# Optimization experiments

Measured on AMD Instinct MI355X. Metric: run time of the kernel, lower is better.

The kernel has to match this reference:

```python
import jax, jax.numpy as jnp
import numpy as np

TEMPERATURE = 0.07
TIME_THRESH = 5.0 * 1e6  # microseconds


def setup_inputs() -> dict:
    key = jax.random.key(0)
    k1, k2, k3 = jax.random.split(key, 3)
    B, D = 8192, 512
    desc = jax.random.normal(k1, (B, D), dtype=jnp.float32)
    desc = desc / jnp.linalg.norm(desc, axis=-1, keepdims=True)  # module expects normalized descriptors
    seq_ids = jax.random.randint(k2, (B,), 0, 64, dtype=jnp.int64)
    time_mid = jax.random.randint(k3, (B,), 0, 20_000_000, dtype=jnp.int64)
    return {"descriptors": desc, "seq_ids": seq_ids, "time_mid": time_mid}


def reference(descriptors, seq_ids, time_mid):
    B = descriptors.shape[0]
    # [B, B] temperature-scaled cosine similarities
    logits = jnp.matmul(descriptors, descriptors.T) / TEMPERATURE

    eye = jnp.eye(B, dtype=bool)
    same_seq = seq_ids[:, None] == seq_ids[None, :]
    close_time = jnp.abs(time_mid[:, None] - time_mid[None, :]).astype(jnp.float32) < TIME_THRESH
    pos_mask = same_seq & close_time & ~eye  # positives
    offdiag = ~eye                            # positives + negatives = denominator support

    # denominator per row i: log sum_{j != i} exp(logits[i, j])
    denom_lse = jax.nn.logsumexp(jnp.where(offdiag, logits, -jnp.inf), axis=1)  # [B]

    # per positive pair (i, j): -log( exp(l_ij) / denom_i ) = denom_lse_i - l_ij
    pair_loss = jnp.where(pos_mask, denom_lse[:, None] - logits, 0.0)
    num_pos = jnp.sum(pos_mask)
    loss = jnp.sum(pair_loss) / jnp.maximum(num_pos, 1).astype(pair_loss.dtype)
    return loss
```

## Files before the change

kernel.cpp:

```cpp
#include <hip/hip_runtime.h>
#include <math.h>

#define TILE 128

typedef __attribute__((ext_vector_type(4))) float f32x4;
typedef __attribute__((ext_vector_type(2))) long long llong2;

#define INV_T    14.285714285714286f
#define K2C      20.60992915f
#define K2C8     0.32203014296875f
#define INV_T64  0.22321428571428573f
#define TIME_THR 5000000

__device__ __forceinline__ unsigned pack_bf16x2(float lo, float hi) {
  unsigned a = __float_as_uint(lo);
  unsigned b = __float_as_uint(hi);
  a = (a + 0x7FFFu + ((a >> 16) & 1u)) >> 16;
  b = (b + 0x7FFFu + ((b >> 16) & 1u)) & 0xFFFF0000u;
  return b | a;
}

__device__ __forceinline__ unsigned f32_to_e4m3(float x) {
  unsigned u = __float_as_uint(x);
  unsigned s = (u >> 24) & 0x80u;
  int e = (int)((u >> 23) & 0xffu) - 127;
  unsigned m = u & 0x7fffffu;
  if (e < -9) return s;
  if (e < -6) {
    int sh = 20 + (-6 - e);
    unsigned full = (1u << 23) | m;
    unsigned q = full >> sh;
    unsigned rem = full & ((1u << sh) - 1u);
    unsigned half = 1u << (sh - 1);
    if (rem > half || (rem == half && (q & 1u))) q++;
    return s | q;
  }
  unsigned q = m >> 20;
  unsigned rem = m & 0xfffffu;
  if (rem > 0x80000u || (rem == 0x80000u && (q & 1u))) q++;
  int ee = e;
  if (q == 8u) { q = 0u; ee++; }
  if (ee > 8 || (ee == 8 && q == 7u)) return s | 0x7eu;
  return s | (unsigned)((ee + 7) << 3) | q;
}

__device__ __forceinline__ void gl_lds16(const void* g, void* l) {
  __builtin_amdgcn_global_load_lds(
      (const __attribute__((address_space(1))) unsigned int*)g,
      (__attribute__((address_space(3))) unsigned int*)l, 16, 0, 0);
}

template <int MODE>
__device__ __forceinline__ void infonce_body(
    const float* __restrict__ desc, const unsigned char* __restrict__ desc8,
    const int* __restrict__ seq, const int* __restrict__ tmid,
    float* __restrict__ p_se, float* __restrict__ p_ps,
    float* __restrict__ p_pc, int B, int D, int NB) {
  __shared__ __align__(16) unsigned char lA8[3][TILE][64];
  __shared__ __align__(16) unsigned char lB8[3][TILE][64];
  __shared__ int mseq_r[TILE], mtim_r[TILE], mseq_c[TILE], mtim_c[TILE];

  const int T = NB * (NB + 1) / 2;
  int t = blockIdx.x;
  if ((T & 7) == 0) t = (t & 7) * (T >> 3) + (t >> 3);
  float fn = (float)NB + 0.5f;
  int r = (int)(fn - sqrtf(fmaxf(fn * fn - 2.0f * (float)t, 0.0f)));
  if (r < 0) r = 0;
  if (r > NB - 1) r = NB - 1;
  auto Sf = [NB](int rr) { return rr * NB - ((rr * (rr - 1)) >> 1); };
  while (r > 0 && Sf(r) > t) --r;
  while (r < NB - 1 && Sf(r + 1) <= t) ++r;
  const int rb = r;
  const int cb = rb + (t - Sf(rb));
  const bool upper = (cb != rb);

  const int row0 = rb * TILE;
  const int col0 = cb * TILE;

  const int tid = threadIdx.x;
  const int l = tid & 63;
  const int w = tid >> 6;
  const int wrow = (w >> 1) << 6;
  const int wcol = (w & 1) << 6;
  const int lr = l & 15;
  const int kg = l >> 4;

  if (tid < TILE) {
    mseq_r[tid] = seq[row0 + tid];
    mtim_r[tid] = tmid[row0 + tid];
    mseq_c[tid] = seq[col0 + tid];
    mtim_c[tid] = tmid[col0 + tid];
  }

  f32x4 acc[4][4];
#pragma unroll
  for (int m = 0; m < 4; ++m)
#pragma unroll
    for (int n = 0; n < 4; ++n) acc[m][n] = (f32x4){0.f, 0.f, 0.f, 0.f};

  const int NT = D >> 6;

  const int sr = tid >> 3;
  const int sc = tid & 7;

  if (MODE == 2) {
    const unsigned char* pa =
        desc8 + (size_t)(row0 + (tid >> 2)) * D + (tid & 3) * 16;
    const unsigned char* pb =
        desc8 + (size_t)(col0 + (tid >> 2)) * D + (tid & 3) * 16;
    const size_t rstep = (size_t)64 * D;

    auto stage = [&](int bu_, int tt) {
      const int off = tt << 6;
      gl_lds16(pa + off, (char*)&lA8[bu_][0][0] + tid * 16);
      gl_lds16(pa + off + rstep, (char*)&lA8[bu_][0][0] + 4096 + tid * 16);
      gl_lds16(pb + off, (char*)&lB8[bu_][0][0] + tid * 16);
      gl_lds16(pb + off + rstep, (char*)&lB8[bu_][0][0] + 4096 + tid * 16);
    };

    __builtin_amdgcn_sched_barrier(0);
    stage(0, 0);
    if (NT > 1) stage(1, 1);
    __builtin_amdgcn_sched_barrier(0);

    int bu = 0;
    for (int ts = 0; ts < NT; ++ts) {
      if (ts + 2 < NT) {
        int sbu = bu + 2;
        if (sbu >= 3) sbu -= 3;
        stage(sbu, ts + 2);
        __builtin_amdgcn_sched_barrier(0);
        asm volatile("s_waitcnt vmcnt(8)" ::: "memory");
      } else if (ts + 1 < NT) {
        asm volatile("s_waitcnt vmcnt(4)" ::: "memory");
      } else {
        asm volatile("s_waitcnt vmcnt(0)" ::: "memory");
      }
      __builtin_amdgcn_sched_barrier(0);
      __builtin_amdgcn_s_barrier();
      __builtin_amdgcn_sched_barrier(0);

      llong2 av[4], bv[4];
#pragma unroll
      for (int m = 0; m < 4; ++m) {
        const int row = wrow + (m << 4) + lr;
        const int ch = kg ^ ((row + (row >> 2)) & 3);
        av[m] = *reinterpret_cast<const llong2*>(&lA8[bu][row][ch << 4]);
      }
#pragma unroll
      for (int n = 0; n < 4; ++n) {
        const int row = wcol + (n << 4) + lr;
        const int ch = kg ^ ((row + (row >> 2)) & 3);
        bv[n] = *reinterpret_cast<const llong2*>(&lB8[bu][row][ch << 4]);
      }
      __builtin_amdgcn_sched_barrier(0);
      asm volatile("s_waitcnt lgkmcnt(0)" ::: "memory");
      __builtin_amdgcn_sched_barrier(0);
      __builtin_amdgcn_s_setprio(1);
#pragma unroll
      for (int kk = 0; kk < 2; ++kk)
#pragma unroll
        for (int m = 0; m < 4; ++m)
#pragma unroll
          for (int n = 0; n < 4; ++n)
            acc[m][n] = __builtin_amdgcn_mfma_f32_16x16x32_fp8_fp8(
                av[m][kk], bv[n][kk], acc[m][n], 0, 0, 0);
      __builtin_amdgcn_s_setprio(0);
      __builtin_amdgcn_sched_barrier(0);
      __builtin_amdgcn_s_barrier();
      bu = bu == 2 ? 0 : bu + 1;
    }
    __syncthreads();
  } else {
    __shared__ __align__(16) unsigned short lAw[TILE][64];
    __shared__ __align__(16) unsigned short lBw[TILE][64];
    typedef __attribute__((ext_vector_type(8))) short short8v;
    for (int k0 = 0; k0 < D; k0 += 64) {
      __syncthreads();
#pragma unroll
      for (int p = 0; p < 4; ++p) {
        const int rr = (p << 5) + sr;
        const float* gA = desc + (size_t)(row0 + rr) * D + k0 + (sc << 3);
        const float4 fa0 = *reinterpret_cast<const float4*>(gA);
        const float4 fa1 = *reinterpret_cast<const float4*>(gA + 4);
        const float* gB = desc + (size_t)(col0 + rr) * D + k0 + (sc << 3);
        const float4 fb0 = *reinterpret_cast<const float4*>(gB);
        const float4 fb1 = *reinterpret_cast<const float4*>(gB + 4);
        uint4 wa, wb;
        wa.x = pack_bf16x2(fa0.x, fa0.y);
        wa.y = pack_bf16x2(fa0.z, fa0.w);
        wa.z = pack_bf16x2(fa1.x, fa1.y);
        wa.w = pack_bf16x2(fa1.z, fa1.w);
        wb.x = pack_bf16x2(fb0.x, fb0.y);
        wb.y = pack_bf16x2(fb0.z, fb0.w);
        wb.z = pack_bf16x2(fb1.x, fb1.y);
        wb.w = pack_bf16x2(fb1.z, fb1.w);
        const int dst = (sc ^ (rr & 7)) << 3;
        *reinterpret_cast<uint4*>(&lAw[rr][dst]) = wa;
        *reinterpret_cast<uint4*>(&lBw[rr][dst]) = wb;
      }
      __syncthreads();
#pragma unroll
      for (int kk = 0; kk < 2; ++kk) {
        short8v af[4], bf[4];
#pragma unroll
        for (int m = 0; m < 4; ++m) {
          const int rowa = wrow + (m << 4) + lr;
          const int ch = ((kk << 2) + kg) ^ (rowa & 7);
          af[m] = *reinterpret_cast<const short8v*>(&lAw[rowa][ch << 3]);
        }
#pragma unroll
        for (int n = 0; n < 4; ++n) {
          const int rowb = wcol + (n << 4) + lr;
          const int ch = ((kk << 2) + kg) ^ (rowb & 7);
          bf[n] = *reinterpret_cast<const short8v*>(&lBw[rowb][ch << 3]);
        }
#pragma unroll
        for (int m = 0; m < 4; ++m)
#pragma unroll
          for (int n = 0; n < 4; ++n)
            acc[m][n] = __builtin_amdgcn_mfma_f32_16x16x32_bf16(af[m], bf[n],
                                                                acc[m][n], 0, 0, 0);
      }
    }
    __syncthreads();
  }

  float* rowred = (float*)&lA8[0][0][0];
  float* colred = (float*)&lB8[0][0][0];

  const float kmul = (MODE == 2) ? K2C8 : K2C;
  const float psc = (MODE == 2) ? INV_T64 : INV_T;

  int cseq[4], ctim[4], gcol[4];
#pragma unroll
  for (int n = 0; n < 4; ++n) {
    const int cl = wcol + (n << 4) + lr;
    cseq[n] = mseq_c[cl];
    ctim[n] = mtim_c[cl];
    gcol[n] = col0 + cl;
  }
  float colse[4] = {0.f, 0.f, 0.f, 0.f};
  float colpd[4] = {0.f, 0.f, 0.f, 0.f};
  float colpc[4] = {0.f, 0.f, 0.f, 0.f};

#pragma unroll
  for (int m = 0; m < 4; ++m) {
#pragma unroll
    for (int reg = 0; reg < 4; ++reg) {
      const int rl = wrow + (m << 4) + (kg << 2) + reg;
      const int growg = row0 + rl;
      const int rs = mseq_r[rl];
      const int rt = mtim_r[rl];
      float se = 0.f, pd = 0.f, pcnt = 0.f;
#pragma unroll
      for (int n = 0; n < 4; ++n) {
        const float dot = acc[m][n][reg];
        const float e = exp2f(fmaf(dot, kmul, -K2C));
        const bool nd = (growg != gcol[n]);
        int dt = rt - ctim[n];
        dt = dt < 0 ? -dt : dt;
        const bool pos = nd && (rs == cseq[n]) && (dt < TIME_THR);
        const float ev = nd ? e : 0.f;
        const float dv = pos ? dot : 0.f;
        const float cv = pos ? 1.f : 0.f;
        se += ev;
        pd += dv;
        pcnt += cv;
        if (upper) {
          colse[n] += ev;
          colpd[n] += dv;
          colpc[n] += cv;
        }
      }
#pragma unroll
      for (int s = 1; s < 16; s <<= 1) {
        se += __shfl_xor(se, s);
        pd += __shfl_xor(pd, s);
        pcnt += __shfl_xor(pcnt, s);
      }
      if ((l & 15) == 0) {
        if (MODE == 2) {
          const int half = wcol >> 6;
          float* rr3 = rowred + ((size_t)(half * TILE + rl)) * 3;
          rr3[0] = se;
          rr3[1] = pd;
          rr3[2] = pcnt;
        } else {
          atomicAdd(&p_se[growg], se);
          atomicAdd(&p_ps[growg], pd * psc);
          atomicAdd(&p_pc[growg], pcnt);
        }
      }
    }
  }
  if (upper) {
#pragma unroll
    for (int n = 0; n < 4; ++n) {
      float cs = colse[n], cp = colpd[n], cc = colpc[n];
      cs += __shfl_xor(cs, 16);
      cp += __shfl_xor(cp, 16);
      cc += __shfl_xor(cc, 16);
      cs += __shfl_xor(cs, 32);
      cp += __shfl_xor(cp, 32);
      cc += __shfl_xor(cc, 32);
      if (kg == 0) {
        if (MODE == 2) {
          const int half = wrow >> 6;
          const int cl = wcol + (n << 4) + lr;
          float* cr3 = colred + ((size_t)(half * TILE + cl)) * 3;
          cr3[0] = cs;
          cr3[1] = cp;
          cr3[2] = cc;
        } else {
          atomicAdd(&p_se[gcol[n]], cs);
          atomicAdd(&p_ps[gcol[n]], cp * psc);
          atomicAdd(&p_pc[gcol[n]], cc);
        }
      }
    }
  }

  if (MODE == 2) {
    __syncthreads();
    if (tid < TILE) {
      const int row = tid;
      const float se = rowred[(size_t)row * 3 + 0] + rowred[(size_t)(TILE + row) * 3 + 0];
      const float pd = rowred[(size_t)row * 3 + 1] + rowred[(size_t)(TILE + row) * 3 + 1];
      const float pc = rowred[(size_t)row * 3 + 2] + rowred[(size_t)(TILE + row) * 3 + 2];
      const size_t o = (size_t)cb * B + row0 + row;
      p_se[o] = se;
      p_ps[o] = pd * INV_T64;
      p_pc[o] = pc;
    } else if (upper && tid < 2 * TILE) {
      const int col = tid - TILE;
      const float se = colred[(size_t)col * 3 + 0] + colred[(size_t)(TILE + col) * 3 + 0];
      const float pd = colred[(size_t)col * 3 + 1] + colred[(size_t)(TILE + col) * 3 + 1];
      const float pc = colred[(size_t)col * 3 + 2] + colred[(size_t)(TILE + col) * 3 + 2];
      const size_t o = (size_t)rb * B + col0 + col;
      p_se[o] = se;
      p_ps[o] = pd * INV_T64;
      p_pc[o] = pc;
    }
  }
}

__global__ __launch_bounds__(256, 2) void infonce_main2(
    const float* desc, const unsigned char* desc8, const int* seq,
    const int* tmid, float* p_se, float* p_ps, float* p_pc, int B, int D,
    int NB) {
  infonce_body<2>(desc, desc8, seq, tmid, p_se, p_ps, p_pc, B, D, NB);
}
__global__ __launch_bounds__(256, 2) void infonce_main0(
    const float* desc, const unsigned char* desc8, const int* seq,
    const int* tmid, float* p_se, float* p_ps, float* p_pc, int B, int D,
    int NB) {
  infonce_body<0>(desc, desc8, seq, tmid, p_se, p_ps, p_pc, B, D, NB);
}

__global__ __launch_bounds__(256) void conv_fp8(const float* __restrict__ in,
                                                unsigned char* __restrict__ out,
                                                int D, int nchunk) {
  const int u = blockIdx.x * 256 + threadIdx.x;
  if (u >= nchunk) return;
  const int cpr = D >> 4;
  const int r = u / cpr;
  const int cc = u - r * cpr;
  const int kb = cc >> 2;
  const int c = cc & 3;
  const int kg = c ^ ((r + (r >> 2)) & 3);
  const float* src = in + (size_t)r * D + kb * 64 + kg * 8;
  const float4 f0 = *reinterpret_cast<const float4*>(src);
  const float4 f1 = *reinterpret_cast<const float4*>(src + 4);
  const float4 g0 = *reinterpret_cast<const float4*>(src + 32);
  const float4 g1 = *reinterpret_cast<const float4*>(src + 36);
  unsigned char b[16];
  b[0] = f32_to_e4m3(f0.x * 8.f);
  b[1] = f32_to_e4m3(f0.y * 8.f);
  b[2] = f32_to_e4m3(f0.z * 8.f);
  b[3] = f32_to_e4m3(f0.w * 8.f);
  b[4] = f32_to_e4m3(f1.x * 8.f);
  b[5] = f32_to_e4m3(f1.y * 8.f);
  b[6] = f32_to_e4m3(f1.z * 8.f);
  b[7] = f32_to_e4m3(f1.w * 8.f);
  b[8] = f32_to_e4m3(g0.x * 8.f);
  b[9] = f32_to_e4m3(g0.y * 8.f);
  b[10] = f32_to_e4m3(g0.z * 8.f);
  b[11] = f32_to_e4m3(g0.w * 8.f);
  b[12] = f32_to_e4m3(g1.x * 8.f);
  b[13] = f32_to_e4m3(g1.y * 8.f);
  b[14] = f32_to_e4m3(g1.z * 8.f);
  b[15] = f32_to_e4m3(g1.w * 8.f);
  uint4 wv;
  unsigned* wp = (unsigned*)&wv;
#pragma unroll
  for (int d = 0; d < 4; ++d)
    wp[d] = (unsigned)b[d * 4] | ((unsigned)b[d * 4 + 1] << 8) |
            ((unsigned)b[d * 4 + 2] << 16) | ((unsigned)b[d * 4 + 3] << 24);
  *reinterpret_cast<uint4*>(out + (size_t)u * 16) = wv;
}

__global__ __launch_bounds__(256) void reduce_parts4(
    const float* __restrict__ p_se, const float* __restrict__ p_ps,
    const float* __restrict__ p_pc, float* __restrict__ bnum,
    float* __restrict__ bcnt, int B, int NB) {
  const int tid = threadIdx.x;
  const int rloc = tid & 63;
  const int chunk = tid >> 6;
  const int row = blockIdx.x * 64 + rloc;
  const int jpc = NB >> 2;
  float se = 0.f, ps = 0.f, pc = 0.f;
  for (int j = chunk * jpc; j < (chunk + 1) * jpc; ++j) {
    const size_t o = (size_t)j * B + row;
    se += p_se[o];
    ps += p_ps[o];
    pc += p_pc[o];
  }
  __shared__ float s3[3][4][64];
  s3[0][chunk][rloc] = se;
  s3[1][chunk][rloc] = ps;
  s3[2][chunk][rloc] = pc;
  __syncthreads();
  if (tid < 64) {
    const float tse = s3[0][0][tid] + s3[0][1][tid] + s3[0][2][tid] + s3[0][3][tid];
    const float tps = s3[1][0][tid] + s3[1][1][tid] + s3[1][2][tid] + s3[1][3][tid];
    const float tpc = s3[2][0][tid] + s3[2][1][tid] + s3[2][2][tid] + s3[2][3][tid];
    float a = tpc * (logf(tse) + INV_T) - tps;
    float b = tpc;
#pragma unroll
    for (int s = 1; s < 64; s <<= 1) {
      a += __shfl_xor(a, s);
      b += __shfl_xor(b, s);
    }
    if (tid == 0) {
      bnum[blockIdx.x] = a;
      bcnt[blockIdx.x] = b;
    }
  }
}

__global__ __launch_bounds__(256) void final_reduce(
    const float* __restrict__ bnum, const float* __restrict__ bcnt,
    float* __restrict__ out, int n) {
  __shared__ float sn[256];
  __shared__ float sc[256];
  const int tid = threadIdx.x;
  float a = 0.f, b = 0.f;
  for (int i = tid; i < n; i += 256) {
    a += bnum[i];
    b += bcnt[i];
  }
  sn[tid] = a;
  sc[tid] = b;
  __syncthreads();
  for (int s = 128; s > 0; s >>= 1) {
    if (tid < s) {
      sn[tid] += sn[tid + s];
      sc[tid] += sc[tid + s];
    }
    __syncthreads();
  }
  if (tid == 0) out[0] = sn[0] / fmaxf(sc[0], 1.f);
}

__global__ __launch_bounds__(1024) void infonce_finalize(
    const float* __restrict__ a_se, const float* __restrict__ a_ps,
    const float* __restrict__ a_pc, float* __restrict__ out, int B) {
  __shared__ float sn[1024];
  __shared__ float sc[1024];
  const int tid = threadIdx.x;
  float num = 0.f, cnt = 0.f;
  for (int i = tid; i < B; i += 1024) {
    const float c = a_pc[i];
    num += c * (logf(a_se[i]) + INV_T) - a_ps[i];
    cnt += c;
  }
  sn[tid] = num;
  sc[tid] = cnt;
  __syncthreads();
  for (int s = 512; s > 0; s >>= 1) {
    if (tid < s) {
      sn[tid] += sn[tid + s];
      sc[tid] += sc[tid + s];
    }
    __syncthreads();
  }
  if (tid == 0) out[0] = sn[0] / fmaxf(sc[0], 1.f);
}

extern "C" void kernel_launch(void* const* d_in, const int* in_sizes, int n_in,
                              void* d_out, int out_size, void* d_ws, size_t ws_size,
                              hipStream_t stream) {
  (void)n_in;
  (void)out_size;
  const float* desc = (const float*)d_in[0];
  const int* seq = (const int*)d_in[1];
  const int* tmid = (const int*)d_in[2];
  const int B = in_sizes[1];
  const int D = in_sizes[0] / B;
  const int NB = B / TILE;
  const int T = NB * (NB + 1) / 2;

  const size_t desc8_bytes = (size_t)B * D;
  const size_t parts_elems = (size_t)B * NB;
  const size_t nb1 = (size_t)B / 64;
  const size_t need8 = desc8_bytes + 3 * parts_elems * 4 + 2 * nb1 * 4;

  if ((B & 255) == 0 && (D & 63) == 0 && ws_size >= need8) {
    unsigned char* desc8 = (unsigned char*)d_ws;
    float* p_se = (float*)((char*)d_ws + desc8_bytes);
    float* p_ps = p_se + parts_elems;
    float* p_pc = p_ps + parts_elems;
    float* bnum = p_pc + parts_elems;
    float* bcnt = bnum + nb1;
    const int nchunk = (int)(((size_t)B * D) >> 4);
    conv_fp8<<<(nchunk + 255) / 256, 256, 0, stream>>>(desc, desc8, D, nchunk);
    infonce_main2<<<T, 256, 0, stream>>>(desc, desc8, seq, tmid, p_se, p_ps,
                                         p_pc, B, D, NB);
    const int nrb = B / 64;
    reduce_parts4<<<nrb, 256, 0, stream>>>(p_se, p_ps, p_pc, bnum, bcnt, B, NB);
    final_reduce<<<1, 256, 0, stream>>>(bnum, bcnt, (float*)d_out, nrb);
  } else {
    float* a_se = (float*)d_ws;
    float* a_ps = a_se + B;
    float* a_pc = a_ps + B;
    hipMemsetAsync(d_ws, 0, (size_t)3 * B * sizeof(float), stream);
    infonce_main0<<<T, 256, 0, stream>>>(desc, nullptr, seq, tmid, a_se, a_ps,
                                         a_pc, B, D, NB);
    infonce_finalize<<<1, 1024, 0, stream>>>(a_se, a_ps, a_pc, (float*)d_out, B);
  }
}
```

Before: 98.74 us.

## Double the FP8 K-tile to 128 and switch to double-buffered LDS staging

Each main-loop iteration now stages a 128-byte K slice per row instead of 64, moving from a triple buffer to a double buffer. The LDS swizzle changes to an XOR over 8 chunks, and the FP8 conversion kernel writes data in that matching layout. With D=512 this halves the iteration count and the number of barriers. The cost is a shallower prefetch (one stage ahead instead of two), which may expose more load latency per iteration.

```diff
diff --git a/kernel.cpp b/kernel.cpp
--- a/kernel.cpp
+++ b/kernel.cpp
@@ -56,8 +56,8 @@
     const int* __restrict__ seq, const int* __restrict__ tmid,
     float* __restrict__ p_se, float* __restrict__ p_ps,
     float* __restrict__ p_pc, int B, int D, int NB) {
-  __shared__ __align__(16) unsigned char lA8[3][TILE][64];
-  __shared__ __align__(16) unsigned char lB8[3][TILE][64];
+  __shared__ __align__(16) unsigned char lA8[2][TILE][128];
+  __shared__ __align__(16) unsigned char lB8[2][TILE][128];
   __shared__ int mseq_r[TILE], mtim_r[TILE], mseq_c[TILE], mtim_c[TILE];
 
   const int T = NB * (NB + 1) / 2;
@@ -98,41 +98,38 @@
 #pragma unroll
     for (int n = 0; n < 4; ++n) acc[m][n] = (f32x4){0.f, 0.f, 0.f, 0.f};
 
-  const int NT = D >> 6;
-
   const int sr = tid >> 3;
   const int sc = tid & 7;
 
   if (MODE == 2) {
+    const int NT = D >> 7;
     const unsigned char* pa =
-        desc8 + (size_t)(row0 + (tid >> 2)) * D + (tid & 3) * 16;
+        desc8 + (size_t)(row0 + (tid >> 3)) * D + (tid & 7) * 16;
     const unsigned char* pb =
-        desc8 + (size_t)(col0 + (tid >> 2)) * D + (tid & 3) * 16;
-    const size_t rstep = (size_t)64 * D;
+        desc8 + (size_t)(col0 + (tid >> 3)) * D + (tid & 7) * 16;
+    const size_t rstep = (size_t)32 * D;
 
     auto stage = [&](int bu_, int tt) {
-      const int off = tt << 6;
-      gl_lds16(pa + off, (char*)&lA8[bu_][0][0] + tid * 16);
-      gl_lds16(pa + off + rstep, (char*)&lA8[bu_][0][0] + 4096 + tid * 16);
-      gl_lds16(pb + off, (char*)&lB8[bu_][0][0] + tid * 16);
-      gl_lds16(pb + off + rstep, (char*)&lB8[bu_][0][0] + 4096 + tid * 16);
+      const int off = tt << 7;
+#pragma unroll
+      for (int q = 0; q < 4; ++q) {
+        gl_lds16(pa + (size_t)q * rstep + off,
+                 (char*)&lA8[bu_][0][0] + (q << 12) + tid * 16);
+        gl_lds16(pb + (size_t)q * rstep + off,
+                 (char*)&lB8[bu_][0][0] + (q << 12) + tid * 16);
+      }
     };
 
     __builtin_amdgcn_sched_barrier(0);
     stage(0, 0);
-    if (NT > 1) stage(1, 1);
     __builtin_amdgcn_sched_barrier(0);
 
-    int bu = 0;
     for (int ts = 0; ts < NT; ++ts) {
-      if (ts + 2 < NT) {
-        int sbu = bu + 2;
-        if (sbu >= 3) sbu -= 3;
-        stage(sbu, ts + 2);
+      const int bu = ts & 1;
+      if (ts + 1 < NT) {
+        stage(bu ^ 1, ts + 1);
         __builtin_amdgcn_sched_barrier(0);
         asm volatile("s_waitcnt vmcnt(8)" ::: "memory");
-      } else if (ts + 1 < NT) {
-        asm volatile("s_waitcnt vmcnt(4)" ::: "memory");
       } else {
         asm volatile("s_waitcnt vmcnt(0)" ::: "memory");
       }
@@ -140,35 +137,44 @@
       __builtin_amdgcn_s_barrier();
       __builtin_amdgcn_sched_barrier(0);
 
-      llong2 av[4], bv[4];
+      llong2 av[4][2], bv[4][2];
 #pragma unroll
       for (int m = 0; m < 4; ++m) {
         const int row = wrow + (m << 4) + lr;
-        const int ch = kg ^ ((row + (row >> 2)) & 3);
-        av[m] = *reinterpret_cast<const llong2*>(&lA8[bu][row][ch << 4]);
+#pragma unroll
+        for (int j2 = 0; j2 < 2; ++j2) {
+          const int ch = ((j2 << 2) + kg) ^ (row & 7);
+          av[m][j2] =
+              *reinterpret_cast<const llong2*>(&lA8[bu][row][ch << 4]);
+        }
       }
 #pragma unroll
       for (int n = 0; n < 4; ++n) {
         const int row = wcol + (n << 4) + lr;
-        const int ch = kg ^ ((row + (row >> 2)) & 3);
-        bv[n] = *reinterpret_cast<const llong2*>(&lB8[bu][row][ch << 4]);
+#pragma unroll
+        for (int j2 = 0; j2 < 2; ++j2) {
+          const int ch = ((j2 << 2) + kg) ^ (row & 7);
+          bv[n][j2] =
+              *reinterpret_cast<const llong2*>(&lB8[bu][row][ch << 4]);
+        }
       }
       __builtin_amdgcn_sched_barrier(0);
       asm volatile("s_waitcnt lgkmcnt(0)" ::: "memory");
       __builtin_amdgcn_sched_barrier(0);
       __builtin_amdgcn_s_setprio(1);
 #pragma unroll
-      for (int kk = 0; kk < 2; ++kk)
-#pragma unroll
-        for (int m = 0; m < 4; ++m)
-#pragma unroll
-          for (int n = 0; n < 4; ++n)
-            acc[m][n] = __builtin_amdgcn_mfma_f32_16x16x32_fp8_fp8(
-                av[m][kk], bv[n][kk], acc[m][n], 0, 0, 0);
+      for (int j2 = 0; j2 < 2; ++j2)
+#pragma unroll
+        for (int kk = 0; kk < 2; ++kk)
+#pragma unroll
+          for (int m = 0; m < 4; ++m)
+#pragma unroll
+            for (int n = 0; n < 4; ++n)
+              acc[m][n] = __builtin_amdgcn_mfma_f32_16x16x32_fp8_fp8(
+                  av[m][j2][kk], bv[n][j2][kk], acc[m][n], 0, 0, 0);
       __builtin_amdgcn_s_setprio(0);
       __builtin_amdgcn_sched_barrier(0);
       __builtin_amdgcn_s_barrier();
-      bu = bu == 2 ? 0 : bu + 1;
     }
     __syncthreads();
   } else {
@@ -366,10 +372,12 @@
   const int cpr = D >> 4;
   const int r = u / cpr;
   const int cc = u - r * cpr;
-  const int kb = cc >> 2;
-  const int c = cc & 3;
-  const int kg = c ^ ((r + (r >> 2)) & 3);
-  const float* src = in + (size_t)r * D + kb * 64 + kg * 8;
+  const int kt = cc >> 3;
+  const int p = cc & 7;
+  const int g = p ^ (r & 7);
+  const int j2 = g >> 2;
+  const int kgc = g & 3;
+  const float* src = in + (size_t)r * D + (kt << 7) + (j2 << 6) + (kgc << 3);
   const float4 f0 = *reinterpret_cast<const float4*>(src);
   const float4 f1 = *reinterpret_cast<const float4*>(src + 4);
   const float4 g0 = *reinterpret_cast<const float4*>(src + 32);
@@ -506,7 +514,7 @@
   const size_t nb1 = (size_t)B / 64;
   const size_t need8 = desc8_bytes + 3 * parts_elems * 4 + 2 * nb1 * 4;
 
-  if ((B & 255) == 0 && (D & 63) == 0 && ws_size >= need8) {
+  if ((B & 255) == 0 && (D & 127) == 0 && ws_size >= need8) {
     unsigned char* desc8 = (unsigned char*)d_ws;
     float* p_se = (float*)((char*)d_ws + desc8_bytes);
     float* p_ps = p_se + parts_elems;
```

Measured after the change: 95.47 us. -3.3%, faster.
